# Optimization experiments

Hardware: AMD Instinct MI355X
Metric: run time of the kernel (lower is better)

Reference implementation:

```python
import jax, jax.numpy as jnp
import numpy as np


def setup_inputs() -> dict:
    key = jax.random.key(0)
    k1, k2 = jax.random.split(key)
    E, D, N = 1600000, 32, 100000
    e = jax.random.normal(k1, (E, D), dtype=jnp.float32)
    dst = jax.random.randint(k2, (E,), 0, N, dtype=jnp.int64)
    return {"e": e, "dst": dst, "n_nodes": N}


def reference(e, dst, n_nodes):
    # copy_e + mean reducer == segment mean of edge features over dst nodes.
    # DGL yields 0 for nodes with no in-edges.
    sums = jax.ops.segment_sum(e, dst, num_segments=n_nodes)          # [N, D]
    counts = jax.ops.segment_sum(jnp.ones((e.shape[0],), e.dtype), dst,
                                 num_segments=n_nodes)                 # [N]
    denom = jnp.maximum(counts, 1.0)[:, None]
    return sums / denom
```

## Files before the change

kernel.cpp:

```cpp
#include <hip/hip_runtime.h>


#define D_FEAT 32
#define NPB 64
#define NB_MAX 2048
#define STAGE 3200
#define CAP_LDS 2048
#define CURSOR_PAD 16

__global__ __launch_bounds__(256) void bin_kernel(
    const int* __restrict__ dst,
    int* __restrict__ cursor,
    unsigned int* __restrict__ buckets,
    int E, int nb, int cap, int chunk)
{
    __shared__ int hist[NB_MAX];
    __shared__ int offs[NB_MAX];
    __shared__ int run [NB_MAX];
    __shared__ int gpos[NB_MAX];
    __shared__ unsigned int   st_rec[STAGE];
    __shared__ unsigned short st_b  [STAGE];
    __shared__ int wsum[4];

    int t = threadIdx.x;
    int cstart = blockIdx.x * chunk;
    int cn = E - cstart; if (cn > chunk) cn = chunk;
    if (cn <= 0) return;

    for (int i = t; i < nb; i += 256) hist[i] = 0;
    __syncthreads();

    int nv = cn >> 2;
    const int4* d4 = (const int4*)(dst + cstart);
    for (int i = t; i < nv; i += 256) {
        int4 d = d4[i];
        atomicAdd(&hist[d.x >> 6], 1);
        atomicAdd(&hist[d.y >> 6], 1);
        atomicAdd(&hist[d.z >> 6], 1);
        atomicAdd(&hist[d.w >> 6], 1);
    }
    for (int i = (nv << 2) + t; i < cn; i += 256)
        atomicAdd(&hist[dst[cstart + i] >> 6], 1);
    __syncthreads();

    int q = (nb + 255) >> 8;
    int lo = t * q, hi = lo + q; if (hi > nb) hi = nb;
    int sum = 0;
    for (int i = lo; i < hi; i++) sum += hist[i];
    int lane = t & 63, w = t >> 6;
    int x = sum;
    for (int off = 1; off < 64; off <<= 1) {
        int y = __shfl_up(x, off, 64);
        if (lane >= off) x += y;
    }
    if (lane == 63) wsum[w] = x;
    __syncthreads();
    int wex = 0;
    for (int u = 0; u < w; u++) wex += wsum[u];
    int ex = wex + x - sum;
    for (int i = lo; i < hi; i++) {
        offs[i] = ex;
        run[i]  = ex;
        ex += hist[i];
    }
    __syncthreads();

    for (int i = t; i < nb; i += 256) {
        int h = hist[i];
        gpos[i] = (h > 0) ? atomicAdd(&cursor[i * CURSOR_PAD], h) : 0;
    }
    __syncthreads();

    for (int i = t; i < nv; i += 256) {
        int4 d = d4[i];
        int g = cstart + (i << 2);
        int b0 = d.x >> 6, b1 = d.y >> 6, b2 = d.z >> 6, b3 = d.w >> 6;
        int p0 = atomicAdd(&run[b0], 1);
        int p1 = atomicAdd(&run[b1], 1);
        int p2 = atomicAdd(&run[b2], 1);
        int p3 = atomicAdd(&run[b3], 1);
        st_rec[p0] = ((unsigned)(g    ) << 6) | (unsigned)(d.x & 63); st_b[p0] = (unsigned short)b0;
        st_rec[p1] = ((unsigned)(g + 1) << 6) | (unsigned)(d.y & 63); st_b[p1] = (unsigned short)b1;
        st_rec[p2] = ((unsigned)(g + 2) << 6) | (unsigned)(d.z & 63); st_b[p2] = (unsigned short)b2;
        st_rec[p3] = ((unsigned)(g + 3) << 6) | (unsigned)(d.w & 63); st_b[p3] = (unsigned short)b3;
    }
    for (int i = (nv << 2) + t; i < cn; i += 256) {
        int g = cstart + i;
        int d = dst[g];
        int b = d >> 6;
        int p = atomicAdd(&run[b], 1);
        st_rec[p] = ((unsigned)g << 6) | (unsigned)(d & 63);
        st_b[p]   = (unsigned short)b;
    }
    __syncthreads();

    for (int p = t; p < cn; p += 256) {
        int b = st_b[p];
        int rel = gpos[b] + (p - offs[b]);
        if (rel < cap)
            buckets[(size_t)b * cap + rel] = st_rec[p];
    }
}

__global__ __launch_bounds__(256) void bucket_gather_kernel(
    const float4* __restrict__ e4,
    const unsigned int* __restrict__ buckets,
    const int* __restrict__ cursor,
    float4* __restrict__ out4,
    int N, int cap)
{
    __shared__ unsigned int st_raw[CAP_LDS];
    __shared__ unsigned int st_ids[CAP_LDS];
    __shared__ int hist[NPB];
    __shared__ int sc  [NPB];
    __shared__ int run [NPB];

    int t = threadIdx.x;
    int b = blockIdx.x;

    if (t < NPB) hist[t] = 0;
    __syncthreads();

    int m = cursor[b * CURSOR_PAD]; if (m > cap) m = cap;
    const unsigned int* rec = buckets + (size_t)b * cap;

    for (int i = t; i < m; i += 256) {
        unsigned r = rec[i];
        st_raw[i] = r;
        atomicAdd(&hist[r & 63], 1);
    }
    __syncthreads();

    if (t < 64) {
        int v = hist[t];
        int x = v;
        for (int off = 1; off < 64; off <<= 1) {
            int y = __shfl_up(x, off, 64);
            if (t >= off) x += y;
        }
        sc[t]  = x - v;
        run[t] = x - v;
    }
    __syncthreads();

    for (int i = t; i < m; i += 256) {
        unsigned r = st_raw[i];
        int p = atomicAdd(&run[r & 63], 1);
        st_ids[p] = r >> 6;
    }
    __syncthreads();

    int g = t >> 3, j = t & 7;
    for (int pass = 0; pass < 2; pass++) {
        int local = pass * 32 + g;
        int node = b * NPB + local;
        int s = sc[local];
        int c = hist[local];
        float4 a0 = {0.f,0.f,0.f,0.f}, a1 = {0.f,0.f,0.f,0.f};
        float4 a2 = {0.f,0.f,0.f,0.f}, a3 = {0.f,0.f,0.f,0.f};
        int k = 0;
        for (; k + 4 <= c; k += 4) {
            unsigned e0 = st_ids[s+k],   e1 = st_ids[s+k+1];
            unsigned e2 = st_ids[s+k+2], e3 = st_ids[s+k+3];
            float4 v0 = e4[(size_t)e0*8 + j];
            float4 v1 = e4[(size_t)e1*8 + j];
            float4 v2 = e4[(size_t)e2*8 + j];
            float4 v3 = e4[(size_t)e3*8 + j];
            a0.x += v0.x; a0.y += v0.y; a0.z += v0.z; a0.w += v0.w;
            a1.x += v1.x; a1.y += v1.y; a1.z += v1.z; a1.w += v1.w;
            a2.x += v2.x; a2.y += v2.y; a2.z += v2.z; a2.w += v2.w;
            a3.x += v3.x; a3.y += v3.y; a3.z += v3.z; a3.w += v3.w;
        }
        for (; k < c; k++) {
            unsigned e0 = st_ids[s+k];
            float4 v0 = e4[(size_t)e0*8 + j];
            a0.x += v0.x; a0.y += v0.y; a0.z += v0.z; a0.w += v0.w;
        }
        if (node < N) {
            float inv = 1.0f / (float)(c > 1 ? c : 1);
            float4 r;
            r.x = (a0.x + a1.x + a2.x + a3.x) * inv;
            r.y = (a0.y + a1.y + a2.y + a3.y) * inv;
            r.z = (a0.z + a1.z + a2.z + a3.z) * inv;
            r.w = (a0.w + a1.w + a2.w + a3.w) * inv;
            out4[(size_t)node * 8 + j] = r;
        }
    }
}

__global__ __launch_bounds__(256) void scatter_atomic_kernel(
    const float4* __restrict__ e4, const int* __restrict__ dst,
    float* __restrict__ sums, int* __restrict__ counts, int total)
{
    int t = blockIdx.x * 256 + threadIdx.x;
    if (t >= total) return;
    int edge = t >> 3;
    int fq = t & 7;
    float4 v = e4[t];
    int d = dst[edge];
    float* o = sums + (size_t)d * D_FEAT + fq * 4;
    atomicAdd(o + 0, v.x);
    atomicAdd(o + 1, v.y);
    atomicAdd(o + 2, v.z);
    atomicAdd(o + 3, v.w);
    if (fq == 0) atomicAdd(counts + d, 1);
}

__global__ __launch_bounds__(256) void finalize_kernel(
    float4* __restrict__ out4, const int* __restrict__ counts, int total)
{
    int t = blockIdx.x * 256 + threadIdx.x;
    if (t >= total) return;
    int node = t >> 3;
    int c = counts[node];
    float inv = 1.0f / (float)(c > 1 ? c : 1);
    float4 v = out4[t];
    v.x *= inv; v.y *= inv; v.z *= inv; v.w *= inv;
    out4[t] = v;
}

extern "C" void kernel_launch(void* const* d_in, const int* in_sizes, int n_in,
                              void* d_out, int out_size, void* d_ws, size_t ws_size,
                              hipStream_t stream) {
    const float4* e4 = (const float4*)d_in[0];
    const int* dst = (const int*)d_in[1];
    int E = in_sizes[0] / D_FEAT;
    int N = out_size / D_FEAT;

    int nb = (N + NPB - 1) / NPB;
    long long avg = (E + nb - 1) / nb;
    long long thresh = avg + 8 * (long long)(__builtin_sqrt((double)avg)) + 64;
    int cap = (int)((thresh + 63) / 64 * 64);

    char* ws = (char*)d_ws;
    size_t fast_need = (size_t)nb * CURSOR_PAD * 4
                     + (size_t)nb * cap * 4;

    if (nb <= NB_MAX && cap <= CAP_LDS && E <= (1 << 25) && ws_size >= fast_need) {
        int* cursor = (int*)ws;
        unsigned int* buckets = (unsigned int*)(ws + (size_t)nb * CURSOR_PAD * 4);

        hipMemsetAsync(cursor, 0, (size_t)nb * CURSOR_PAD * 4, stream);

        int chunk = (E + 511) / 512;
        chunk = (chunk + 3) & ~3;
        if (chunk > STAGE) chunk = STAGE & ~3;
        int grid1 = (E + chunk - 1) / chunk;
        bin_kernel<<<grid1, 256, 0, stream>>>(dst, cursor, buckets, E, nb, cap, chunk);
        bucket_gather_kernel<<<nb, 256, 0, stream>>>(e4, buckets, cursor,
                                                     (float4*)d_out, N, cap);
    } else {
        int* counts = (int*)ws;
        hipMemsetAsync(d_out, 0, (size_t)out_size * sizeof(float), stream);
        hipMemsetAsync(counts, 0, (size_t)N * 4, stream);
        int total = E * (D_FEAT / 4);
        scatter_atomic_kernel<<<(total + 255) / 256, 256, 0, stream>>>(
            e4, dst, (float*)d_out, counts, total);
        int fin = N * (D_FEAT / 4);
        finalize_kernel<<<(fin + 255) / 256, 256, 0, stream>>>(
            (float4*)d_out, counts, fin);
    }
}
```

Before: 347.7 us.

## Widen buckets to 128 nodes and balance gather with edge-sliced LDS atomics

Doubles the number of nodes per bucket, halving the bucket count. In the gather kernel, each 8-thread group now takes an equal slice of the sorted edge list instead of whole nodes, and flushes run-length partial sums into an LDS sum table with atomics. This is meant to remove load imbalance from variable node degree and raise occupancy. The bin kernel also rotates the starting bucket per block so global cursor atomics are spread out, at the cost of extra LDS atomics and a larger LDS footprint.

```diff
diff --git a/kernel.cpp b/kernel.cpp
--- a/kernel.cpp
+++ b/kernel.cpp
@@ -2,13 +2,13 @@
 
 
 #define D_FEAT 32
-#define NPB 64
-#define NB_MAX 2048
+#define NPB 128
+#define NB_MAX 1024
 #define STAGE 3200
-#define CAP_LDS 2048
+#define CAP_LDS 2560
 #define CURSOR_PAD 16
 
-__global__ __launch_bounds__(256) void bin_kernel(
+__global__ __launch_bounds__(256, 4) void bin_kernel(
     const int* __restrict__ dst,
     int* __restrict__ cursor,
     unsigned int* __restrict__ buckets,
@@ -34,13 +34,13 @@
     const int4* d4 = (const int4*)(dst + cstart);
     for (int i = t; i < nv; i += 256) {
         int4 d = d4[i];
-        atomicAdd(&hist[d.x >> 6], 1);
-        atomicAdd(&hist[d.y >> 6], 1);
-        atomicAdd(&hist[d.z >> 6], 1);
-        atomicAdd(&hist[d.w >> 6], 1);
+        atomicAdd(&hist[d.x >> 7], 1);
+        atomicAdd(&hist[d.y >> 7], 1);
+        atomicAdd(&hist[d.z >> 7], 1);
+        atomicAdd(&hist[d.w >> 7], 1);
     }
     for (int i = (nv << 2) + t; i < cn; i += 256)
-        atomicAdd(&hist[dst[cstart + i] >> 6], 1);
+        atomicAdd(&hist[dst[cstart + i] >> 7], 1);
     __syncthreads();
 
     int q = (nb + 255) >> 8;
@@ -65,31 +65,33 @@
     }
     __syncthreads();
 
+    int off0 = (blockIdx.x * 199) % nb;
     for (int i = t; i < nb; i += 256) {
-        int h = hist[i];
-        gpos[i] = (h > 0) ? atomicAdd(&cursor[i * CURSOR_PAD], h) : 0;
+        int ii = i + off0; if (ii >= nb) ii -= nb;
+        int h = hist[ii];
+        gpos[ii] = (h > 0) ? atomicAdd(&cursor[ii * CURSOR_PAD], h) : 0;
     }
     __syncthreads();
 
     for (int i = t; i < nv; i += 256) {
         int4 d = d4[i];
         int g = cstart + (i << 2);
-        int b0 = d.x >> 6, b1 = d.y >> 6, b2 = d.z >> 6, b3 = d.w >> 6;
+        int b0 = d.x >> 7, b1 = d.y >> 7, b2 = d.z >> 7, b3 = d.w >> 7;
         int p0 = atomicAdd(&run[b0], 1);
         int p1 = atomicAdd(&run[b1], 1);
         int p2 = atomicAdd(&run[b2], 1);
         int p3 = atomicAdd(&run[b3], 1);
-        st_rec[p0] = ((unsigned)(g    ) << 6) | (unsigned)(d.x & 63); st_b[p0] = (unsigned short)b0;
-        st_rec[p1] = ((unsigned)(g + 1) << 6) | (unsigned)(d.y & 63); st_b[p1] = (unsigned short)b1;
-        st_rec[p2] = ((unsigned)(g + 2) << 6) | (unsigned)(d.z & 63); st_b[p2] = (unsigned short)b2;
-        st_rec[p3] = ((unsigned)(g + 3) << 6) | (unsigned)(d.w & 63); st_b[p3] = (unsigned short)b3;
+        st_rec[p0] = ((unsigned)(g    ) << 7) | (unsigned)(d.x & 127); st_b[p0] = (unsigned short)b0;
+        st_rec[p1] = ((unsigned)(g + 1) << 7) | (unsigned)(d.y & 127); st_b[p1] = (unsigned short)b1;
+        st_rec[p2] = ((unsigned)(g + 2) << 7) | (unsigned)(d.z & 127); st_b[p2] = (unsigned short)b2;
+        st_rec[p3] = ((unsigned)(g + 3) << 7) | (unsigned)(d.w & 127); st_b[p3] = (unsigned short)b3;
     }
     for (int i = (nv << 2) + t; i < cn; i += 256) {
         int g = cstart + i;
         int d = dst[g];
-        int b = d >> 6;
+        int b = d >> 7;
         int p = atomicAdd(&run[b], 1);
-        st_rec[p] = ((unsigned)g << 6) | (unsigned)(d & 63);
+        st_rec[p] = ((unsigned)g << 7) | (unsigned)(d & 127);
         st_b[p]   = (unsigned short)b;
     }
     __syncthreads();
@@ -102,7 +104,7 @@
     }
 }
 
-__global__ __launch_bounds__(256) void bucket_gather_kernel(
+__global__ __launch_bounds__(256, 4) void bucket_gather_kernel(
     const float4* __restrict__ e4,
     const unsigned int* __restrict__ buckets,
     const int* __restrict__ cursor,
@@ -110,15 +112,16 @@
     int N, int cap)
 {
     __shared__ unsigned int st_raw[CAP_LDS];
-    __shared__ unsigned int st_ids[CAP_LDS];
+    __shared__ unsigned int st_srt[CAP_LDS];
+    __shared__ float sums[NPB][33];
     __shared__ int hist[NPB];
-    __shared__ int sc  [NPB];
     __shared__ int run [NPB];
 
     int t = threadIdx.x;
     int b = blockIdx.x;
 
-    if (t < NPB) hist[t] = 0;
+    for (int i = t; i < NPB; i += 256) hist[i] = 0;
+    for (int i = t; i < NPB * 33; i += 256) ((float*)sums)[i] = 0.f;
     __syncthreads();
 
     int m = cursor[b * CURSOR_PAD]; if (m > cap) m = cap;
@@ -127,63 +130,110 @@
     for (int i = t; i < m; i += 256) {
         unsigned r = rec[i];
         st_raw[i] = r;
-        atomicAdd(&hist[r & 63], 1);
+        atomicAdd(&hist[r & 127], 1);
     }
     __syncthreads();
 
     if (t < 64) {
-        int v = hist[t];
-        int x = v;
+        int v0 = hist[2 * t], v1 = hist[2 * t + 1];
+        int s = v0 + v1;
+        int x = s;
         for (int off = 1; off < 64; off <<= 1) {
             int y = __shfl_up(x, off, 64);
             if (t >= off) x += y;
         }
-        sc[t]  = x - v;
-        run[t] = x - v;
+        int ex = x - s;
+        run[2 * t]     = ex;
+        run[2 * t + 1] = ex + v0;
     }
     __syncthreads();
 
     for (int i = t; i < m; i += 256) {
         unsigned r = st_raw[i];
-        int p = atomicAdd(&run[r & 63], 1);
-        st_ids[p] = r >> 6;
+        int p = atomicAdd(&run[r & 127], 1);
+        st_srt[p] = r;
     }
     __syncthreads();
 
     int g = t >> 3, j = t & 7;
-    for (int pass = 0; pass < 2; pass++) {
-        int local = pass * 32 + g;
+    int slice = (m + 31) >> 5;
+    int s0 = g * slice;
+    int s1 = s0 + slice; if (s1 > m) s1 = m;
+    float* srow = &sums[0][0] + j * 4;
+    float4 acc = {0.f, 0.f, 0.f, 0.f};
+    int cur = -1;
+    int k = s0;
+    for (; k + 4 <= s1; k += 4) {
+        unsigned r0 = st_srt[k], r1 = st_srt[k+1], r2 = st_srt[k+2], r3 = st_srt[k+3];
+        float4 v0 = e4[(size_t)(r0 >> 7) * 8 + j];
+        float4 v1 = e4[(size_t)(r1 >> 7) * 8 + j];
+        float4 v2 = e4[(size_t)(r2 >> 7) * 8 + j];
+        float4 v3 = e4[(size_t)(r3 >> 7) * 8 + j];
+        int l0 = r0 & 127, l1 = r1 & 127, l2 = r2 & 127, l3 = r3 & 127;
+        if (l0 != cur) {
+            if (cur >= 0) {
+                float* p = srow + cur * 33;
+                atomicAdd(p + 0, acc.x); atomicAdd(p + 1, acc.y);
+                atomicAdd(p + 2, acc.z); atomicAdd(p + 3, acc.w);
+            }
+            acc.x = acc.y = acc.z = acc.w = 0.f; cur = l0;
+        }
+        acc.x += v0.x; acc.y += v0.y; acc.z += v0.z; acc.w += v0.w;
+        if (l1 != cur) {
+            float* p = srow + cur * 33;
+            atomicAdd(p + 0, acc.x); atomicAdd(p + 1, acc.y);
+            atomicAdd(p + 2, acc.z); atomicAdd(p + 3, acc.w);
+            acc.x = acc.y = acc.z = acc.w = 0.f; cur = l1;
+        }
+        acc.x += v1.x; acc.y += v1.y; acc.z += v1.z; acc.w += v1.w;
+        if (l2 != cur) {
+            float* p = srow + cur * 33;
+            atomicAdd(p + 0, acc.x); atomicAdd(p + 1, acc.y);
+            atomicAdd(p + 2, acc.z); atomicAdd(p + 3, acc.w);
+            acc.x = acc.y = acc.z = acc.w = 0.f; cur = l2;
+        }
+        acc.x += v2.x; acc.y += v2.y; acc.z += v2.z; acc.w += v2.w;
+        if (l3 != cur) {
+            float* p = srow + cur * 33;
+            atomicAdd(p + 0, acc.x); atomicAdd(p + 1, acc.y);
+            atomicAdd(p + 2, acc.z); atomicAdd(p + 3, acc.w);
+            acc.x = acc.y = acc.z = acc.w = 0.f; cur = l3;
+        }
+        acc.x += v3.x; acc.y += v3.y; acc.z += v3.z; acc.w += v3.w;
+    }
+    for (; k < s1; k++) {
+        unsigned r0 = st_srt[k];
+        float4 v0 = e4[(size_t)(r0 >> 7) * 8 + j];
+        int l0 = r0 & 127;
+        if (l0 != cur) {
+            if (cur >= 0) {
+                float* p = srow + cur * 33;
+                atomicAdd(p + 0, acc.x); atomicAdd(p + 1, acc.y);
+                atomicAdd(p + 2, acc.z); atomicAdd(p + 3, acc.w);
+            }
+            acc.x = acc.y = acc.z = acc.w = 0.f; cur = l0;
+        }
+        acc.x += v0.x; acc.y += v0.y; acc.z += v0.z; acc.w += v0.w;
+    }
+    if (cur >= 0) {
+        float* p = srow + cur * 33;
+        atomicAdd(p + 0, acc.x); atomicAdd(p + 1, acc.y);
+        atomicAdd(p + 2, acc.z); atomicAdd(p + 3, acc.w);
+    }
+    __syncthreads();
+
+    for (int s = t; s < NPB * 8; s += 256) {
+        int local = s >> 3, jj = s & 7;
         int node = b * NPB + local;
-        int s = sc[local];
-        int c = hist[local];
-        float4 a0 = {0.f,0.f,0.f,0.f}, a1 = {0.f,0.f,0.f,0.f};
-        float4 a2 = {0.f,0.f,0.f,0.f}, a3 = {0.f,0.f,0.f,0.f};
-        int k = 0;
-        for (; k + 4 <= c; k += 4) {
-            unsigned e0 = st_ids[s+k],   e1 = st_ids[s+k+1];
-            unsigned e2 = st_ids[s+k+2], e3 = st_ids[s+k+3];
-            float4 v0 = e4[(size_t)e0*8 + j];
-            float4 v1 = e4[(size_t)e1*8 + j];
-            float4 v2 = e4[(size_t)e2*8 + j];
-            float4 v3 = e4[(size_t)e3*8 + j];
-            a0.x += v0.x; a0.y += v0.y; a0.z += v0.z; a0.w += v0.w;
-            a1.x += v1.x; a1.y += v1.y; a1.z += v1.z; a1.w += v1.w;
-            a2.x += v2.x; a2.y += v2.y; a2.z += v2.z; a2.w += v2.w;
-            a3.x += v3.x; a3.y += v3.y; a3.z += v3.z; a3.w += v3.w;
-        }
-        for (; k < c; k++) {
-            unsigned e0 = st_ids[s+k];
-            float4 v0 = e4[(size_t)e0*8 + j];
-            a0.x += v0.x; a0.y += v0.y; a0.z += v0.z; a0.w += v0.w;
-        }
         if (node < N) {
+            int c = hist[local];
             float inv = 1.0f / (float)(c > 1 ? c : 1);
             float4 r;
-            r.x = (a0.x + a1.x + a2.x + a3.x) * inv;
-            r.y = (a0.y + a1.y + a2.y + a3.y) * inv;
-            r.z = (a0.z + a1.z + a2.z + a3.z) * inv;
-            r.w = (a0.w + a1.w + a2.w + a3.w) * inv;
-            out4[(size_t)node * 8 + j] = r;
+            r.x = sums[local][jj * 4 + 0] * inv;
+            r.y = sums[local][jj * 4 + 1] * inv;
+            r.z = sums[local][jj * 4 + 2] * inv;
+            r.w = sums[local][jj * 4 + 3] * inv;
+            out4[(size_t)node * 8 + jj] = r;
         }
     }
 }
```

After: 335.3 us. -3.6%, faster.
